# Optimization experiments

Measured on AMD Instinct MI355X. Metric: run time of the kernel, lower is better.

The kernel has to match this reference:

```python
import jax, jax.numpy as jnp
import numpy as np

B, T, D, H, L = 32, 2048, 256, 256, 2  # batch, seq, input, hidden, layers


def setup_inputs() -> dict:
    key = jax.random.key(0)
    ks = jax.random.split(key, 5)
    s = 1.0 / np.sqrt(H)  # torch GRU uniform(-1/sqrt(H), 1/sqrt(H)) scale
    return {
        "x": jax.random.normal(ks[0], (B, T, D), dtype=jnp.float32),
        "W_ih": jax.random.uniform(ks[1], (L, 3 * H, D), jnp.float32, -s, s),
        "W_hh": jax.random.uniform(ks[2], (L, 3 * H, H), jnp.float32, -s, s),
        "b_ih": jax.random.uniform(ks[3], (L, 3 * H), jnp.float32, -s, s),
        "b_hh": jax.random.uniform(ks[4], (L, 3 * H), jnp.float32, -s, s),
    }


def _gru_layer(x_btd, W_ih_l, W_hh_l, b_ih_l, b_hh_l, h0_bh):
    # Precompute input projections for the whole sequence: [B,T,3H]
    x_proj = jnp.einsum("btd,gd->btg", x_btd, W_ih_l) + b_ih_l
    x_proj_t = jnp.swapaxes(x_proj, 0, 1)  # [T,B,3H] for scan over time

    def step(h, xp):
        hp = h @ W_hh_l.T + b_hh_l  # [B,3H]
        xr, xz, xn = jnp.split(xp, 3, axis=-1)
        hr, hz, hn = jnp.split(hp, 3, axis=-1)
        r = jax.nn.sigmoid(xr + hr)
        z = jax.nn.sigmoid(xz + hz)
        n = jnp.tanh(xn + r * hn)
        h_new = (1.0 - z) * n + z * h
        return h_new, h_new

    _, ys = jax.lax.scan(step, h0_bh, x_proj_t)  # ys: [T,B,H]
    return jnp.swapaxes(ys, 0, 1)  # [B,T,H]


def reference(x, W_ih, W_hh, b_ih, b_hh):
    # h0 = ones, matching the torch module's hidden_0 = ones(...)
    h0 = jnp.ones((x.shape[0], H), dtype=x.dtype)
    out = x
    for l in range(L):  # small fixed layer count
        out = _gru_layer(out, W_ih[l], W_hh[l], b_ih[l], b_hh[l], h0)
    return out
```

## Files before the change

kernel.cpp:

```cpp
#include <hip/hip_runtime.h>

typedef _Float16 h2 __attribute__((ext_vector_type(2)));
typedef _Float16 h8 __attribute__((ext_vector_type(8)));
typedef float f4 __attribute__((ext_vector_type(4)));

__global__ void cvt_f32_f16(const float* __restrict__ s, _Float16* __restrict__ d, int n) {
    int i = blockIdx.x * blockDim.x + threadIdx.x;
    if (i < n) d[i] = (_Float16)s[i];
}

template<bool AF16>
__global__ __launch_bounds__(256, 2) void gemm_xproj(
    const void* __restrict__ Ap, const _Float16* __restrict__ Bt,
    const float* __restrict__ bias, float* __restrict__ C)
{
    __shared__ __align__(16) _Float16 As[128 * 40];
    __shared__ __align__(16) _Float16 Bs[128 * 40];
    const int tid = threadIdx.x;
    const size_t m0 = (size_t)blockIdx.x * 128;
    const int n0 = blockIdx.y * 128;
    const int lane = tid & 63, wave = tid >> 6;
    const int wm = wave >> 1, wn = wave & 1;
    const int r16 = lane & 15, kg = lane >> 4;
    f4 acc[4][4] = {};
    for (int k0 = 0; k0 < 256; k0 += 32) {
        if (k0) __syncthreads();
        #pragma unroll
        for (int u = 0; u < 2; ++u) {
            int c = tid + u * 256;
            int row = c >> 2, off = (c & 3) * 8;
            h8 av;
            if constexpr (AF16) {
                av = *(const h8*)((const _Float16*)Ap + (m0 + row) * 256 + k0 + off);
            } else {
                const float* ap = (const float*)Ap + (m0 + row) * 256 + k0 + off;
                f4 f0 = *(const f4*)ap, f1 = *(const f4*)(ap + 4);
                av[0]=(_Float16)f0[0]; av[1]=(_Float16)f0[1]; av[2]=(_Float16)f0[2]; av[3]=(_Float16)f0[3];
                av[4]=(_Float16)f1[0]; av[5]=(_Float16)f1[1]; av[6]=(_Float16)f1[2]; av[7]=(_Float16)f1[3];
            }
            *(h8*)&As[row * 40 + off] = av;
            h8 bv = *(const h8*)(Bt + (size_t)(n0 + row) * 256 + k0 + off);
            *(h8*)&Bs[row * 40 + off] = bv;
        }
        __syncthreads();
        h8 af[4], bf[4];
        #pragma unroll
        for (int mi = 0; mi < 4; ++mi) af[mi] = *(const h8*)&As[(wm*64 + mi*16 + r16) * 40 + kg * 8];
        #pragma unroll
        for (int ni = 0; ni < 4; ++ni) bf[ni] = *(const h8*)&Bs[(wn*64 + ni*16 + r16) * 40 + kg * 8];
        #pragma unroll
        for (int mi = 0; mi < 4; ++mi)
            #pragma unroll
            for (int ni = 0; ni < 4; ++ni)
                acc[mi][ni] = __builtin_amdgcn_mfma_f32_16x16x32_f16(af[mi], bf[ni], acc[mi][ni], 0, 0, 0);
    }
    #pragma unroll
    for (int mi = 0; mi < 4; ++mi)
        #pragma unroll
        for (int ni = 0; ni < 4; ++ni) {
            int col = n0 + wn*64 + ni*16 + r16;
            float bv = bias[col];
            #pragma unroll
            for (int r = 0; r < 4; ++r) {
                int row = wm*64 + mi*16 + kg*4 + r;
                C[(m0 + row) * 768 + col] = acc[mi][ni][r] + bv;
            }
        }
}

template<bool OUTF32>
__global__ __launch_bounds__(512, 2) void gru_scan(
    const float* __restrict__ xp,
    const _Float16* __restrict__ Whh,
    const float* __restrict__ bhh,
    float* __restrict__ o32,
    _Float16* __restrict__ o16)
{
    __shared__ __align__(16) float    hf[2][256];
    __shared__ __align__(16) _Float16 hh[2][256];
    const int b = blockIdx.x;
    const int tid = threadIdx.x;
    const int j = tid >> 1, hlf = tid & 1;

    h2 wr[64], wz[64], wn[64];
    {
        const h8* p0 = (const h8*)(Whh + (size_t)j * 256 + hlf * 128);
        const h8* p1 = (const h8*)(Whh + (size_t)(j + 256) * 256 + hlf * 128);
        const h8* p2 = (const h8*)(Whh + (size_t)(j + 512) * 256 + hlf * 128);
        #pragma unroll
        for (int k8 = 0; k8 < 16; ++k8) {
            h8 v0 = p0[k8]; __builtin_memcpy(&wr[k8 * 4], &v0, 16);
            h8 v1 = p1[k8]; __builtin_memcpy(&wz[k8 * 4], &v1, 16);
            h8 v2 = p2[k8]; __builtin_memcpy(&wn[k8 * 4], &v2, 16);
        }
    }
    const float br = bhh[j], bz = bhh[j + 256], bn = bhh[j + 512];
    if (tid < 256) { hf[0][tid] = 1.0f; hh[0][tid] = (_Float16)1.0f; }
    __syncthreads();

    const float* xb = xp + (size_t)b * 2048 * 768;
    float xr = xb[j], xz = xb[j + 256], xn = xb[j + 512];
    int cur = 0;
    for (int t = 0; t < 2048; ++t) {
        const float* xnx = xb + (size_t)(t + 1 < 2048 ? t + 1 : t) * 768;
        float pr = xnx[j], pz = xnx[j + 256], pn = xnx[j + 512];

        float ar = 0.f, az = 0.f, an = 0.f;
        const h8* hv8 = (const h8*)&hh[cur][hlf * 128];
        #pragma unroll
        for (int k8 = 0; k8 < 16; ++k8) {
            h8 hc = hv8[k8];
            h2 hp[4]; __builtin_memcpy(&hp, &hc, 16);
            #pragma unroll
            for (int q = 0; q < 4; ++q) {
                int k = k8 * 4 + q;
                ar = __builtin_amdgcn_fdot2(wr[k], hp[q], ar, false);
                az = __builtin_amdgcn_fdot2(wz[k], hp[q], az, false);
                an = __builtin_amdgcn_fdot2(wn[k], hp[q], an, false);
            }
        }
        ar += __shfl_xor(ar, 1);
        az += __shfl_xor(az, 1);
        an += __shfl_xor(an, 1);

        float rg = 1.f / (1.f + __expf(-(xr + ar + br)));
        float zg = 1.f / (1.f + __expf(-(xz + az + bz)));
        float narg = xn + rg * (an + bn);
        float aa = fabsf(narg);
        float e = __expf(-2.f * aa);
        float ng = copysignf((1.f - e) / (1.f + e), narg);
        float hold = hf[cur][j];
        float hnew = (1.f - zg) * ng + zg * hold;

        const int nxt = cur ^ 1;
        if (hlf == 0) {
            hf[nxt][j] = hnew;
            hh[nxt][j] = (_Float16)hnew;
            size_t oi = ((size_t)b * 2048 + t) * 256 + j;
            if constexpr (OUTF32) o32[oi] = hnew; else o16[oi] = (_Float16)hnew;
        }
        __syncthreads();
        cur = nxt;
        xr = pr; xz = pz; xn = pn;
    }
}

extern "C" void kernel_launch(void* const* d_in, const int* in_sizes, int n_in,
                              void* d_out, int out_size, void* d_ws, size_t ws_size,
                              hipStream_t stream) {
    const float* x    = (const float*)d_in[0];
    const float* W_ih = (const float*)d_in[1];
    const float* W_hh = (const float*)d_in[2];
    const float* b_ih = (const float*)d_in[3];
    const float* b_hh = (const float*)d_in[4];
    float* out = (float*)d_out;

    char* ws = (char*)d_ws;
    float*     xproj = (float*)ws;
    _Float16*  Wih_h = (_Float16*)(ws + 201326592);
    _Float16*  Whh_h = (_Float16*)(ws + 201326592 + 786432);
    _Float16*  y1h   = (_Float16*)(ws + 201326592 + 2 * 786432);

    cvt_f32_f16<<<1536, 256, 0, stream>>>(W_ih, Wih_h, 393216);
    cvt_f32_f16<<<1536, 256, 0, stream>>>(W_hh, Whh_h, 393216);

    gemm_xproj<false><<<dim3(512, 6), 256, 0, stream>>>(x, Wih_h, b_ih, xproj);
    gru_scan<false><<<32, 512, 0, stream>>>(xproj, Whh_h, b_hh, nullptr, y1h);

    gemm_xproj<true><<<dim3(512, 6), 256, 0, stream>>>(y1h, Wih_h + 196608, b_ih + 768, xproj);
    gru_scan<true><<<32, 512, 0, stream>>>(xproj, Whh_h + 196608, b_hh + 768, out, nullptr);
}
```

Baseline: 5.076 ms.

## Use MFMA for recurrent matvec and fold r/z hidden biases into projection

The recurrent h·W_hh^T per timestep moves from per-thread fdot2 loops to 16x16x32 MFMA instructions. Each wave keeps a 32-column slice of all three gates' weights in registers, and the hidden state is broadcast as the A operand, so only row 0 of each result is used. The r and z hidden biases are folded into the input-projection bias by a small prep kernel, the fp32 h copy in shared memory is replaced by per-lane registers, and x-projection prefetch is deepened to two steps. The aim is a shorter per-step latency on the serial critical path. The cost is that 15 of 16 MFMA rows are wasted, and register pressure from the 48 h8 weight fragments is high.

Measured after the change: 6.378 ms. 1.26x slower.

```diff
diff --git a/kernel.cpp b/kernel.cpp
--- a/kernel.cpp
+++ b/kernel.cpp
@@ -7,6 +7,17 @@
 __global__ void cvt_f32_f16(const float* __restrict__ s, _Float16* __restrict__ d, int n) {
     int i = blockIdx.x * blockDim.x + threadIdx.x;
     if (i < n) d[i] = (_Float16)s[i];
+}
+
+__global__ void prep_bias(const float* __restrict__ bih, const float* __restrict__ bhh,
+                          float* __restrict__ b2, int n) {
+    int i = blockIdx.x * blockDim.x + threadIdx.x;
+    if (i < n) {
+        int c = i % 768;
+        float v = bih[i];
+        if (c < 512) v += bhh[i];
+        b2[i] = v;
+    }
 }
 
 template<bool AF16>
@@ -69,79 +80,94 @@
 }
 
 template<bool OUTF32>
-__global__ __launch_bounds__(512, 2) void gru_scan(
+__global__
+__attribute__((amdgpu_flat_work_group_size(512, 512), amdgpu_waves_per_eu(2, 2)))
+void gru_scan_mfma(
     const float* __restrict__ xp,
     const _Float16* __restrict__ Whh,
     const float* __restrict__ bhh,
     float* __restrict__ o32,
     _Float16* __restrict__ o16)
 {
-    __shared__ __align__(16) float    hf[2][256];
     __shared__ __align__(16) _Float16 hh[2][256];
-    const int b = blockIdx.x;
-    const int tid = threadIdx.x;
-    const int j = tid >> 1, hlf = tid & 1;
-
-    h2 wr[64], wz[64], wn[64];
-    {
-        const h8* p0 = (const h8*)(Whh + (size_t)j * 256 + hlf * 128);
-        const h8* p1 = (const h8*)(Whh + (size_t)(j + 256) * 256 + hlf * 128);
-        const h8* p2 = (const h8*)(Whh + (size_t)(j + 512) * 256 + hlf * 128);
-        #pragma unroll
-        for (int k8 = 0; k8 < 16; ++k8) {
-            h8 v0 = p0[k8]; __builtin_memcpy(&wr[k8 * 4], &v0, 16);
-            h8 v1 = p1[k8]; __builtin_memcpy(&wz[k8 * 4], &v1, 16);
-            h8 v2 = p2[k8]; __builtin_memcpy(&wn[k8 * 4], &v2, 16);
-        }
-    }
-    const float br = bhh[j], bz = bhh[j + 256], bn = bhh[j + 512];
-    if (tid < 256) { hf[0][tid] = 1.0f; hh[0][tid] = (_Float16)1.0f; }
+    const int b = blockIdx.x, tid = threadIdx.x;
+    const int w = tid >> 6, lane = tid & 63;
+    const int l15 = lane & 15, kg = lane >> 4;
+    const int j0 = 32 * w;
+
+    h8 Bf[3][2][8];
+    #pragma unroll
+    for (int g = 0; g < 3; ++g)
+        #pragma unroll
+        for (int nt = 0; nt < 2; ++nt) {
+            const _Float16* rp = Whh + (size_t)(g * 256 + j0 + nt * 16 + l15) * 256 + kg * 8;
+            #pragma unroll
+            for (int kk = 0; kk < 8; ++kk)
+                Bf[g][nt][kk] = *(const h8*)(rp + kk * 32);
+        }
+
+    const float bn0 = bhh[512 + j0 + l15];
+    const float bn1 = bhh[512 + j0 + 16 + l15];
+    if (tid < 256) hh[0][tid] = (_Float16)1.0f;
+    float hp0 = 1.0f, hp1 = 1.0f;
     __syncthreads();
 
     const float* xb = xp + (size_t)b * 2048 * 768;
-    float xr = xb[j], xz = xb[j + 256], xn = xb[j + 512];
+    int xoff[6];
+    float c0[6], c1[6];
+    #pragma unroll
+    for (int u = 0; u < 6; ++u) {
+        xoff[u] = (u >> 1) * 256 + j0 + (u & 1) * 16 + l15;
+        c0[u] = xb[xoff[u]];
+        c1[u] = xb[768 + xoff[u]];
+    }
+
     int cur = 0;
     for (int t = 0; t < 2048; ++t) {
-        const float* xnx = xb + (size_t)(t + 1 < 2048 ? t + 1 : t) * 768;
-        float pr = xnx[j], pz = xnx[j + 256], pn = xnx[j + 512];
-
-        float ar = 0.f, az = 0.f, an = 0.f;
-        const h8* hv8 = (const h8*)&hh[cur][hlf * 128];
-        #pragma unroll
-        for (int k8 = 0; k8 < 16; ++k8) {
-            h8 hc = hv8[k8];
-            h2 hp[4]; __builtin_memcpy(&hp, &hc, 16);
-            #pragma unroll
-            for (int q = 0; q < 4; ++q) {
-                int k = k8 * 4 + q;
-                ar = __builtin_amdgcn_fdot2(wr[k], hp[q], ar, false);
-                az = __builtin_amdgcn_fdot2(wz[k], hp[q], az, false);
-                an = __builtin_amdgcn_fdot2(wn[k], hp[q], an, false);
-            }
-        }
-        ar += __shfl_xor(ar, 1);
-        az += __shfl_xor(az, 1);
-        an += __shfl_xor(an, 1);
-
-        float rg = 1.f / (1.f + __expf(-(xr + ar + br)));
-        float zg = 1.f / (1.f + __expf(-(xz + az + bz)));
-        float narg = xn + rg * (an + bn);
-        float aa = fabsf(narg);
-        float e = __expf(-2.f * aa);
-        float ng = copysignf((1.f - e) / (1.f + e), narg);
-        float hold = hf[cur][j];
-        float hnew = (1.f - zg) * ng + zg * hold;
+        const float* xnx = xb + (size_t)((t + 2 < 2048) ? t + 2 : 2047) * 768;
+        float p2[6];
+        #pragma unroll
+        for (int u = 0; u < 6; ++u) p2[u] = xnx[xoff[u]];
+
+        const _Float16* hc = hh[cur];
+        f4 D[6] = {};
+        #pragma unroll
+        for (int kk = 0; kk < 8; ++kk) {
+            h8 A = *(const h8*)(hc + kk * 32 + kg * 8);
+            D[0] = __builtin_amdgcn_mfma_f32_16x16x32_f16(A, Bf[0][0][kk], D[0], 0, 0, 0);
+            D[1] = __builtin_amdgcn_mfma_f32_16x16x32_f16(A, Bf[0][1][kk], D[1], 0, 0, 0);
+            D[2] = __builtin_amdgcn_mfma_f32_16x16x32_f16(A, Bf[1][0][kk], D[2], 0, 0, 0);
+            D[3] = __builtin_amdgcn_mfma_f32_16x16x32_f16(A, Bf[1][1][kk], D[3], 0, 0, 0);
+            D[4] = __builtin_amdgcn_mfma_f32_16x16x32_f16(A, Bf[2][0][kk], D[4], 0, 0, 0);
+            D[5] = __builtin_amdgcn_mfma_f32_16x16x32_f16(A, Bf[2][1][kk], D[5], 0, 0, 0);
+        }
+
+        float rg0 = 1.f / (1.f + __expf(-(c0[0] + D[0][0])));
+        float rg1 = 1.f / (1.f + __expf(-(c0[1] + D[1][0])));
+        float zg0 = 1.f / (1.f + __expf(-(c0[2] + D[2][0])));
+        float zg1 = 1.f / (1.f + __expf(-(c0[3] + D[3][0])));
+        float na0 = c0[4] + rg0 * (D[4][0] + bn0);
+        float na1 = c0[5] + rg1 * (D[5][0] + bn1);
+        float e0 = __expf(-2.f * fabsf(na0));
+        float e1 = __expf(-2.f * fabsf(na1));
+        float ng0 = copysignf((1.f - e0) / (1.f + e0), na0);
+        float ng1 = copysignf((1.f - e1) / (1.f + e1), na1);
+        float hn0 = (1.f - zg0) * ng0 + zg0 * hp0;
+        float hn1 = (1.f - zg1) * ng1 + zg1 * hp1;
+        hp0 = hn0; hp1 = hn1;
 
         const int nxt = cur ^ 1;
-        if (hlf == 0) {
-            hf[nxt][j] = hnew;
-            hh[nxt][j] = (_Float16)hnew;
-            size_t oi = ((size_t)b * 2048 + t) * 256 + j;
-            if constexpr (OUTF32) o32[oi] = hnew; else o16[oi] = (_Float16)hnew;
+        if (kg == 0) {
+            hh[nxt][j0 + l15]      = (_Float16)hn0;
+            hh[nxt][j0 + 16 + l15] = (_Float16)hn1;
+            size_t oi = ((size_t)b * 2048 + t) * 256 + j0 + l15;
+            if constexpr (OUTF32) { o32[oi] = hn0; o32[oi + 16] = hn1; }
+            else                  { o16[oi] = (_Float16)hn0; o16[oi + 16] = (_Float16)hn1; }
         }
         __syncthreads();
         cur = nxt;
-        xr = pr; xz = pz; xn = pn;
+        #pragma unroll
+        for (int u = 0; u < 6; ++u) { c0[u] = c1[u]; c1[u] = p2[u]; }
     }
 }
 
@@ -160,13 +186,15 @@
     _Float16*  Wih_h = (_Float16*)(ws + 201326592);
     _Float16*  Whh_h = (_Float16*)(ws + 201326592 + 786432);
     _Float16*  y1h   = (_Float16*)(ws + 201326592 + 2 * 786432);
+    float*     bias2 = (float*)(ws + 201326592 + 2 * 786432 + 33554432);
 
     cvt_f32_f16<<<1536, 256, 0, stream>>>(W_ih, Wih_h, 393216);
     cvt_f32_f16<<<1536, 256, 0, stream>>>(W_hh, Whh_h, 393216);
-
-    gemm_xproj<false><<<dim3(512, 6), 256, 0, stream>>>(x, Wih_h, b_ih, xproj);
-    gru_scan<false><<<32, 512, 0, stream>>>(xproj, Whh_h, b_hh, nullptr, y1h);
-
-    gemm_xproj<true><<<dim3(512, 6), 256, 0, stream>>>(y1h, Wih_h + 196608, b_ih + 768, xproj);
-    gru_scan<true><<<32, 512, 0, stream>>>(xproj, Whh_h + 196608, b_hh + 768, out, nullptr);
-}
+    prep_bias<<<6, 256, 0, stream>>>(b_ih, b_hh, bias2, 1536);
+
+    gemm_xproj<false><<<dim3(512, 6), 256, 0, stream>>>(x, Wih_h, bias2, xproj);
+    gru_scan_mfma<false><<<32, 512, 0, stream>>>(xproj, Whh_h, b_hh, nullptr, y1h);
+
+    gemm_xproj<true><<<dim3(512, 6), 256, 0, stream>>>(y1h, Wih_h + 196608, bias2 + 768, xproj);
+    gru_scan_mfma<true><<<32, 512, 0, stream>>>(xproj, Whh_h + 196608, b_hh + 768, out, nullptr);
+}
```
